# Kernel tuning notes

Hardware: AMD Instinct MI355X
Metric: run time of the kernel (lower is better)

## Reference

```python
import jax, jax.numpy as jnp
import numpy as np

CAL_W, BF_W, PCP_W, CX_W = 1.0, 1.0, 0.5, 0.5
LIQ_SCALE, EPS = 1.0, 1e-6
BIG = 1e30


def setup_inputs() -> dict:
    n_mat, n_str, W = 32, 256, 4
    N = n_mat * n_str
    rng = np.random.default_rng(0)
    lm = np.tile(np.linspace(-0.5, 0.5, n_str, dtype=np.float32), n_mat)
    tenor = np.repeat(np.linspace(0.02, 2.0, n_mat, dtype=np.float32), n_str)
    cp = (rng.random(N) > 0.5).astype(np.float32)
    geometry = np.stack([lm, tenor, cp], axis=1)
    liquidity = rng.standard_normal((N, 4)).astype(np.float32)
    predicted_iv = (0.1 + 0.5 * rng.random((N, 1))).astype(np.float32)
    node_embeddings = rng.standard_normal((N, 256)).astype(np.float32)
    node = np.arange(N, dtype=np.int32).reshape(n_mat, n_str)
    src_s, dst_s = [], []
    for k in range(1, W + 1):  # strikes k apart within each maturity
        src_s.append(node[:, :-k].ravel()); dst_s.append(node[:, k:].ravel())
    edge_index_strike = np.stack([np.concatenate(src_s), np.concatenate(dst_s)])
    edge_index_maturity = np.stack([node[:-1].ravel(), node[1:].ravel()])
    return {
        'node_embeddings': jnp.asarray(node_embeddings),
        'predicted_iv': jnp.asarray(predicted_iv),
        'geometry': jnp.asarray(geometry),
        'liquidity': jnp.asarray(liquidity),
        'edge_index_strike': jnp.asarray(edge_index_strike),
        'edge_index_maturity': jnp.asarray(edge_index_maturity),
        'max_degree': 2 * W,
    }


def _padded_neighbors(edge_index, N, D):
    # CSR-style padded neighbor lists: row i = all undirected neighbors of i, -1 pad.
    src, dst = edge_index[0], edge_index[1]
    owners = jnp.concatenate([src, dst])
    nbrs = jnp.concatenate([dst, src])
    order = jnp.argsort(owners)  # jax sort is stable -> preserves [dst|src] order
    own_s, nbr_s = owners[order], nbrs[order]
    start = jnp.searchsorted(own_s, jnp.arange(N, dtype=own_s.dtype))
    rank = jnp.arange(own_s.shape[0], dtype=jnp.int32) - start[own_s].astype(jnp.int32)
    return jnp.full((N, D), -1, dtype=jnp.int32).at[own_s, rank].set(nbr_s.astype(jnp.int32))


def _forward(node_embeddings, predicted_iv, geometry, liquidity, edge_index_strike, edge_index_maturity, max_degree):
    lm, tenor, cp = geometry[:, 0], geometry[:, 1], geometry[:, 2]
    lw = jax.nn.sigmoid(liquidity[:, 3] * LIQ_SCALE)
    tv = predicted_iv[:, 0] ** 2 * jnp.maximum(tenor, EPS)  # total variance w = iv^2 * tau
    N = lm.shape[0]
    is_call = cp > 0.5

    # --- calendar arbitrage: total variance nondecreasing in tenor over maturity edges
    ms, md = edge_index_maturity[0], edge_index_maturity[1]
    cvalid = tenor[ms] < tenor[md] - EPS
    cviol = jax.nn.relu(tv[ms] - tv[md])
    cw = jnp.minimum(lw[ms], lw[md])
    ncal = cvalid.sum()
    calendar = jnp.where(ncal > 0, jnp.where(cvalid, cw * cviol, 0.0).sum() / jnp.maximum(ncal, 1), 0.0)

    # --- padded call-neighborhoods over strike edges, sorted by log-moneyness
    nbr = _padded_neighbors(edge_index_strike, N, max_degree)  # [N, D]
    nbr_safe = jnp.maximum(nbr, 0)
    nvalid = (nbr >= 0) & is_call[nbr_safe]
    key = jnp.where(nvalid, lm[nbr_safe], jnp.inf)  # invalid entries pushed to the end
    order = jnp.argsort(key, axis=1)
    ns = jnp.take_along_axis(nbr_safe, order, axis=1)
    vs = jnp.take_along_axis(nvalid, order, axis=1)
    n1, n2, n3 = ns[:, :-2], ns[:, 1:-1], ns[:, 2:]  # consecutive sorted triplets
    trip = vs[:, 2:] & is_call[:, None]  # triplet fully valid iff 3rd slot valid
    lm1, lm2, lm3 = lm[n1], lm[n2], lm[n3]
    denom = lm3 - lm1 + EPS
    alpha = (lm3 - lm2) / denom
    beta = (lm2 - lm1) / denom
    w_pair = lw[:, None] * lw[n2]
    tcount = trip.sum()

    # --- butterfly: interpolated total variance must not exceed the middle node's
    bviol = jax.nn.relu(alpha * tv[n1] + beta * tv[n3] - tv[n2])
    butterfly = jnp.where(tcount > 0, jnp.where(trip, w_pair * bviol, 0.0).sum() / jnp.maximum(tcount, 1), 0.0)

    # --- convexity on embedding norms
    en = jnp.linalg.norm(node_embeddings, axis=1)
    xviol = jax.nn.relu(en[n2] - (alpha * en[n1] + (1.0 - alpha) * en[n3]))
    convexity = jnp.where(tcount > 0, jnp.where(trip, w_pair * xviol, 0.0).sum() / jnp.maximum(tcount, 1), 0.0)

    # --- put-call parity: nearest put in (lm, tenor) per call, sum-sq embedding dist
    is_put = cp < 0.5
    dist = (lm[:, None] - lm[None, :]) ** 2 + (tenor[:, None] - tenor[None, :]) ** 2  # [N, N]
    dist = jnp.where(is_put[None, :], dist, BIG)
    best = jnp.argmin(dist, axis=1)
    emb_d = jnp.sum((node_embeddings - node_embeddings[best]) ** 2, axis=1)
    n_calls, n_puts = is_call.sum(), is_put.sum()
    pcp = jnp.where((n_calls > 0) & (n_puts > 0),
                    jnp.where(is_call, lw * lw[best] * emb_d, 0.0).sum() / jnp.maximum(n_calls, 1), 0.0)

    total = CAL_W * calendar + BF_W * butterfly + PCP_W * pcp + CX_W * convexity
    # order matches the module's dict: calendar, butterfly, put_call, convexity, total
    return jnp.stack([calendar, butterfly, pcp, convexity, total])


def reference(node_embeddings, predicted_iv, geometry, liquidity, edge_index_strike, edge_index_maturity, max_degree):
    return _forward(node_embeddings, predicted_iv, geometry, liquidity, edge_index_strike, edge_index_maturity, max_degree)
```

## Files before the change

kernel.cpp:

```cpp
#include <hip/hip_runtime.h>
#include <math.h>

#define EPS 1e-6f
#define DMAX 8
#define HALFW (DMAX / 2)
#define PREB 1024
#define NSTR 256
#define TAG 0x5A7E0000u
typedef unsigned long long ull;

__device__ __forceinline__ float waveSumF(float v) {
    #pragma unroll
    for (int m = 1; m < 64; m <<= 1) v += __shfl_xor(v, m, 64);
    return v;
}
__device__ __forceinline__ int waveSumI(int v) {
    #pragma unroll
    for (int m = 1; m < 64; m <<= 1) v += __shfl_xor(v, m, 64);
    return v;
}
__device__ __forceinline__ float sigmoidf(float x) {
    return 1.0f / (1.0f + expf(-x));
}

__global__ void k_pre(const float* __restrict__ emb, const float* __restrict__ iv,
                      const float* __restrict__ geom, const float* __restrict__ liq,
                      const int* __restrict__ es, const int* __restrict__ em,
                      float* lwA, float* tvA, float* lmA, float* enA, int* cpA, int* nbr,
                      float* calPartF, int* calPartI, int* ncPart, int* npPart,
                      int* bestj,
                      int N, int ED, int Es, int Em, int n_mat) {
    const int lane = threadIdx.x & 63;

    if ((int)blockIdx.x < PREB) {
        const int tid = blockIdx.x * 256 + threadIdx.x;
        const int gsz = PREB * 256;

        int ic = 0, ip = 0;
        for (int i = tid; i < N; i += gsz) {
            float lm = geom[3*i], ten = geom[3*i+1], cp = geom[3*i+2];
            lmA[i] = lm;
            int c = (cp > 0.5f) ? 1 : 0;
            ic += c; ip += (cp < 0.5f) ? 1 : 0;
            cpA[i] = c;
            lwA[i] = sigmoidf(liq[4*i+3]);
            float v = iv[i];
            tvA[i] = v * v * fmaxf(ten, EPS);
        }

        const int wid = tid >> 6, nw = gsz >> 6, ED4 = ED >> 2;
        for (int r = wid; r < N; r += nw) {
            const float4* row = (const float4*)(emb + (size_t)r * ED);
            float s = 0.f;
            for (int t = lane; t < ED4; t += 64) {
                float4 a = row[t];
                s += a.x*a.x + a.y*a.y + a.z*a.z + a.w*a.w;
            }
            s = waveSumF(s);
            if (lane == 0) enA[r] = sqrtf(s);
        }

        float c = 0.f; int n = 0;
        for (int e = tid; e < Em; e += gsz) {
            int s = em[e], d = em[Em + e];
            float ts = geom[3*s+1], td = geom[3*d+1];
            if (ts < td - EPS) {
                n++;
                float ivs = iv[s], ivd = iv[d];
                float tvs = ivs*ivs*fmaxf(ts, EPS), tvd = ivd*ivd*fmaxf(td, EPS);
                float lws = sigmoidf(liq[4*s+3]), lwd = sigmoidf(liq[4*d+3]);
                c += fminf(lws, lwd) * fmaxf(tvs - tvd, 0.f);
            }
        }
        for (int e = tid; e < Es; e += gsz) {
            int s = es[e], d = es[Es + e];
            int k = d - s;
            if (k >= 1 && k <= HALFW) {
                nbr[s * DMAX + (HALFW + k - 1)] = (int)(TAG | (unsigned)d);
                nbr[d * DMAX + (HALFW - k)]     = (int)(TAG | (unsigned)s);
            }
        }

        __shared__ float sf[4];
        __shared__ int si[4][3];
        c = waveSumF(c); n = waveSumI(n);
        int sc = waveSumI(ic), sp = waveSumI(ip);
        int w = threadIdx.x >> 6;
        if (lane == 0) { sf[w] = c; si[w][0] = n; si[w][1] = sc; si[w][2] = sp; }
        __syncthreads();
        if (threadIdx.x == 0) {
            calPartF[blockIdx.x] = sf[0]+sf[1]+sf[2]+sf[3];
            calPartI[blockIdx.x] = si[0][0]+si[1][0]+si[2][0]+si[3][0];
            ncPart[blockIdx.x]   = si[0][1]+si[1][1]+si[2][1]+si[3][1];
            npPart[blockIdx.x]   = si[0][2]+si[1][2]+si[2][2]+si[3][2];
        }
        return;
    }

    __shared__ float colD2[NSTR];
    __shared__ int   colJ[NSTR];
    __shared__ float colLm[NSTR];
    const int m = (int)blockIdx.x - PREB;
    const int t = threadIdx.x;

    float tm = geom[3*(m*NSTR + t) + 1];
    float bD2 = INFINITY; int bJ = 0; float bLm = 0.f;
    for (int mp = 0; mp < n_mat; ++mp) {
        int j = mp*NSTR + t;
        float lj = geom[3*j], tj = geom[3*j+1], cp = geom[3*j+2];
        float dt = tm - tj;
        float d2 = __fmul_rn(dt, dt);
        if (cp < 0.5f && d2 < bD2) { bD2 = d2; bJ = j; bLm = lj; }
    }
    colD2[t] = bD2; colJ[t] = bJ; colLm[t] = bLm;
    __syncthreads();

    const int i = m*NSTR + t;
    float lmi = geom[3*i];
    ull bestkey = ~0ULL;
    for (int sp = 0; sp < NSTR; ++sp) {
        float dl = lmi - colLm[sp];
        float d  = __fadd_rn(__fmul_rn(dl, dl), colD2[sp]);
        ull key = ((ull)__float_as_uint(d) << 32) | (unsigned)colJ[sp];
        if (key < bestkey) bestkey = key;
    }
    bestj[i] = (int)(bestkey & 0xffffffffULL);
}

__global__ void k_post(const float* __restrict__ emb, const int* __restrict__ bestj,
                       const int* __restrict__ cpA, const float* __restrict__ lwA,
                       const float* __restrict__ tvA, const float* __restrict__ lmA,
                       const float* __restrict__ enA, const int* __restrict__ nbr,
                       float* pcpPart, float* bfPart, float* cxPart, int* tcPart,
                       int N, int ED, int nPcp) {
    __shared__ float sblk[4];
    __shared__ float sblk2[4];
    __shared__ int   sblkI[4];
    const int lane = threadIdx.x & 63;
    const int w    = threadIdx.x >> 6;

    if ((int)blockIdx.x < nPcp) {
        const int i = (blockIdx.x * 256 + threadIdx.x) >> 6;
        const int ED4 = ED >> 2;
        float contrib = 0.f;
        if (i < N && cpA[i]) {
            int b = bestj[i];
            const float4* ri = (const float4*)(emb + (size_t)i * ED);
            const float4* rb = (const float4*)(emb + (size_t)b * ED);
            float s = 0.f;
            for (int t = lane; t < ED4; t += 64) {
                float4 a = ri[t], c = rb[t];
                float dx = a.x-c.x, dy = a.y-c.y, dz = a.z-c.z, dw = a.w-c.w;
                s += dx*dx + dy*dy + dz*dz + dw*dw;
            }
            s = waveSumF(s);
            contrib = lwA[i] * lwA[b] * s;
        }
        if (lane == 0) sblk[w] = contrib;
        __syncthreads();
        if (threadIdx.x == 0)
            pcpPart[blockIdx.x] = sblk[0]+sblk[1]+sblk[2]+sblk[3];
    } else {
        int bb = (int)blockIdx.x - nPcp;
        int i = bb * 256 + threadIdx.x;
        float bf = 0.f, cx = 0.f; int tc = 0;
        if (i < N) {
            int ids[DMAX]; float key[DMAX]; int mv = 0;
            for (int slot = 0; slot < DMAX; slot++) {
                unsigned v = (unsigned)nbr[i * DMAX + slot];
                if ((v & 0xFFFF0000u) == TAG) {
                    int nb = (int)(v & 0xFFFFu);
                    if (cpA[nb]) {
                        float kk = lmA[nb];
                        int p = mv++;
                        while (p > 0 && key[p-1] > kk) { key[p] = key[p-1]; ids[p] = ids[p-1]; p--; }
                        key[p] = kk; ids[p] = nb;
                    }
                }
            }
            if (cpA[i] && mv >= 3) {
                float lwi = lwA[i];
                for (int j = 0; j + 2 < mv; j++) {
                    int n1 = ids[j], n2 = ids[j+1], n3 = ids[j+2];
                    float lm1 = key[j], lm2 = key[j+1], lm3 = key[j+2];
                    float denom = lm3 - lm1 + EPS;
                    float alpha = (lm3 - lm2) / denom;
                    float beta  = (lm2 - lm1) / denom;
                    float bviol = fmaxf(alpha * tvA[n1] + beta * tvA[n3] - tvA[n2], 0.f);
                    float xviol = fmaxf(enA[n2] - (alpha * enA[n1] + (1.0f - alpha) * enA[n3]), 0.f);
                    float wgt = lwi * lwA[n2];
                    bf += wgt * bviol; cx += wgt * xviol; tc++;
                }
            }
        }
        bf = waveSumF(bf); cx = waveSumF(cx); tc = waveSumI(tc);
        if (lane == 0) { sblk[w] = bf; sblk2[w] = cx; sblkI[w] = tc; }
        __syncthreads();
        if (threadIdx.x == 0) {
            bfPart[bb] = sblk[0]+sblk[1]+sblk[2]+sblk[3];
            cxPart[bb] = sblk2[0]+sblk2[1]+sblk2[2]+sblk2[3];
            tcPart[bb] = sblkI[0]+sblkI[1]+sblkI[2]+sblkI[3];
        }
    }
}

__global__ void k_fin(const float* __restrict__ calPartF, const int* __restrict__ calPartI,
                      const int* __restrict__ ncPart, const int* __restrict__ npPart,
                      const float* __restrict__ pcpPart, const float* __restrict__ bfPart,
                      const float* __restrict__ cxPart, const int* __restrict__ tcPart,
                      float* out, int nPcp, int nBtf) {
    const int lane = threadIdx.x & 63;
    const int w    = threadIdx.x >> 6;
    float cs = 0.f, ps = 0.f, bs = 0.f, xs = 0.f;
    int cc = 0, ncall = 0, nput = 0, ts = 0;
    for (int t = threadIdx.x; t < PREB; t += 256) {
        cs += calPartF[t]; cc += calPartI[t]; ncall += ncPart[t]; nput += npPart[t];
    }
    for (int t = threadIdx.x; t < nPcp; t += 256) ps += pcpPart[t];
    for (int t = threadIdx.x; t < nBtf; t += 256) {
        bs += bfPart[t]; xs += cxPart[t]; ts += tcPart[t];
    }
    cs = waveSumF(cs); ps = waveSumF(ps); bs = waveSumF(bs); xs = waveSumF(xs);
    cc = waveSumI(cc); ncall = waveSumI(ncall); nput = waveSumI(nput); ts = waveSumI(ts);
    __shared__ float fcs[4], fps[4], fbs[4], fxs[4];
    __shared__ int   fcc[4], fnc[4], fnp[4], fts[4];
    if (lane == 0) {
        fcs[w] = cs; fps[w] = ps; fbs[w] = bs; fxs[w] = xs;
        fcc[w] = cc; fnc[w] = ncall; fnp[w] = nput; fts[w] = ts;
    }
    __syncthreads();
    if (threadIdx.x == 0) {
        float calSum = fcs[0]+fcs[1]+fcs[2]+fcs[3];
        float pcpSum = fps[0]+fps[1]+fps[2]+fps[3];
        float bfSum  = fbs[0]+fbs[1]+fbs[2]+fbs[3];
        float cxSum  = fxs[0]+fxs[1]+fxs[2]+fxs[3];
        int   calCnt = fcc[0]+fcc[1]+fcc[2]+fcc[3];
        int   nCalls = fnc[0]+fnc[1]+fnc[2]+fnc[3];
        int   nPuts  = fnp[0]+fnp[1]+fnp[2]+fnp[3];
        int   tcount = fts[0]+fts[1]+fts[2]+fts[3];
        float cal = (calCnt > 0) ? calSum / (float)max(calCnt, 1) : 0.f;
        float bf  = (tcount > 0) ? bfSum / (float)tcount : 0.f;
        float cx  = (tcount > 0) ? cxSum / (float)tcount : 0.f;
        float pcp = (nCalls > 0 && nPuts > 0) ? pcpSum / (float)max(nCalls, 1) : 0.f;
        out[0] = cal; out[1] = bf; out[2] = pcp; out[3] = cx;
        out[4] = cal + bf + 0.5f * pcp + 0.5f * cx;
    }
}

extern "C" void kernel_launch(void* const* d_in, const int* in_sizes, int n_in,
                              void* d_out, int out_size, void* d_ws, size_t ws_size,
                              hipStream_t stream) {
    const float* emb  = (const float*)d_in[0];
    const float* iv   = (const float*)d_in[1];
    const float* geom = (const float*)d_in[2];
    const float* liq  = (const float*)d_in[3];
    const int*   es   = (const int*)d_in[4];
    const int*   em   = (const int*)d_in[5];

    const int N  = in_sizes[1];
    const int ED = in_sizes[0] / N;
    const int Es = in_sizes[4] / 2;
    const int Em = in_sizes[5] / 2;
    const int n_mat = N / NSTR;

    const int nPcp = (N + 3) / 4;
    const int nBtf = (N + 255) / 256;

    float* calPartF = (float*)d_ws;
    int*   calPartI = (int*)d_ws + PREB;
    int*   ncPart   = calPartI + PREB;
    int*   npPart   = ncPart + PREB;
    float* pcpPart  = (float*)(npPart + PREB);
    float* bfPart   = pcpPart + nPcp;
    float* cxPart   = bfPart + nBtf;
    int*   tcPart   = (int*)(cxPart + nBtf);
    float* lwA      = (float*)(tcPart + nBtf);
    float* tvA      = lwA + N;
    float* lmA      = tvA + N;
    float* enA      = lmA + N;
    int*   cpA      = (int*)(enA + N);
    int*   nbr      = cpA + N;
    int*   bestj    = nbr + (size_t)DMAX * N;

    k_pre<<<PREB + n_mat, 256, 0, stream>>>(
        emb, iv, geom, liq, es, em,
        lwA, tvA, lmA, enA, cpA, nbr,
        calPartF, calPartI, ncPart, npPart, bestj,
        N, ED, Es, Em, n_mat);

    k_post<<<nPcp + nBtf, 256, 0, stream>>>(
        emb, bestj, cpA, lwA, tvA, lmA, enA, nbr,
        pcpPart, bfPart, cxPart, tcPart, N, ED, nPcp);

    k_fin<<<1, 256, 0, stream>>>(
        calPartF, calPartI, ncPart, npPart, pcpPart, bfPart, cxPart, tcPart,
        (float*)d_out, nPcp, nBtf);
}
```

Before: 98.57 us.

## Fuse final reduction into post kernel via last-block ticket and shrink grids

Removes the separate single-block finalize kernel and instead has the last block of the post kernel, chosen through an atomic ticket counter, perform the global reduction and write the outputs. The counter is zeroed inside the pre kernel. The put-call parity stage now uses a fixed grid of 256 blocks that loop over nodes grid-stride, instead of one wave per node with about 2048 blocks, and the pre kernel's block count is halved. This saves one kernel launch and shrinks the partial arrays, at the cost of an atomic, memory fences and less parallelism per stage.

```diff
diff --git a/kernel.cpp b/kernel.cpp
--- a/kernel.cpp
+++ b/kernel.cpp
@@ -4,7 +4,8 @@
 #define EPS 1e-6f
 #define DMAX 8
 #define HALFW (DMAX / 2)
-#define PREB 1024
+#define PREB 512
+#define PCPB 256
 #define NSTR 256
 #define TAG 0x5A7E0000u
 typedef unsigned long long ull;
@@ -28,13 +29,15 @@
                       const int* __restrict__ es, const int* __restrict__ em,
                       float* lwA, float* tvA, float* lmA, float* enA, int* cpA, int* nbr,
                       float* calPartF, int* calPartI, int* ncPart, int* npPart,
-                      int* bestj,
+                      int* bestj, int* acc,
                       int N, int ED, int Es, int Em, int n_mat) {
     const int lane = threadIdx.x & 63;
 
     if ((int)blockIdx.x < PREB) {
         const int tid = blockIdx.x * 256 + threadIdx.x;
         const int gsz = PREB * 256;
+
+        if (blockIdx.x == 0 && threadIdx.x < 16) acc[threadIdx.x] = 0;
 
         int ic = 0, ip = 0;
         for (int i = tid; i < N; i += gsz) {
@@ -131,37 +134,43 @@
                        const int* __restrict__ cpA, const float* __restrict__ lwA,
                        const float* __restrict__ tvA, const float* __restrict__ lmA,
                        const float* __restrict__ enA, const int* __restrict__ nbr,
+                       const float* __restrict__ calPartF, const int* __restrict__ calPartI,
+                       const int* __restrict__ ncPart, const int* __restrict__ npPart,
                        float* pcpPart, float* bfPart, float* cxPart, int* tcPart,
-                       int N, int ED, int nPcp) {
+                       int* acc, float* out, int N, int ED, int nBtf) {
     __shared__ float sblk[4];
     __shared__ float sblk2[4];
     __shared__ int   sblkI[4];
+    __shared__ int   sticket;
     const int lane = threadIdx.x & 63;
     const int w    = threadIdx.x >> 6;
 
-    if ((int)blockIdx.x < nPcp) {
-        const int i = (blockIdx.x * 256 + threadIdx.x) >> 6;
+    if ((int)blockIdx.x < PCPB) {
+        const int gw = (blockIdx.x * 256 + threadIdx.x) >> 6;
+        const int nw = PCPB * 4;
         const int ED4 = ED >> 2;
-        float contrib = 0.f;
-        if (i < N && cpA[i]) {
-            int b = bestj[i];
-            const float4* ri = (const float4*)(emb + (size_t)i * ED);
-            const float4* rb = (const float4*)(emb + (size_t)b * ED);
-            float s = 0.f;
-            for (int t = lane; t < ED4; t += 64) {
-                float4 a = ri[t], c = rb[t];
-                float dx = a.x-c.x, dy = a.y-c.y, dz = a.z-c.z, dw = a.w-c.w;
-                s += dx*dx + dy*dy + dz*dz + dw*dw;
-            }
-            s = waveSumF(s);
-            contrib = lwA[i] * lwA[b] * s;
-        }
-        if (lane == 0) sblk[w] = contrib;
+        float wacc = 0.f;
+        for (int i = gw; i < N; i += nw) {
+            if (cpA[i]) {
+                int b = bestj[i];
+                const float4* ri = (const float4*)(emb + (size_t)i * ED);
+                const float4* rb = (const float4*)(emb + (size_t)b * ED);
+                float s = 0.f;
+                for (int t = lane; t < ED4; t += 64) {
+                    float4 a = ri[t], c = rb[t];
+                    float dx = a.x-c.x, dy = a.y-c.y, dz = a.z-c.z, dw = a.w-c.w;
+                    s += dx*dx + dy*dy + dz*dz + dw*dw;
+                }
+                s = waveSumF(s);
+                wacc += lwA[i] * lwA[b] * s;
+            }
+        }
+        if (lane == 0) sblk[w] = wacc;
         __syncthreads();
         if (threadIdx.x == 0)
             pcpPart[blockIdx.x] = sblk[0]+sblk[1]+sblk[2]+sblk[3];
     } else {
-        int bb = (int)blockIdx.x - nPcp;
+        int bb = (int)blockIdx.x - PCPB;
         int i = bb * 256 + threadIdx.x;
         float bf = 0.f, cx = 0.f; int tc = 0;
         if (i < N) {
@@ -202,48 +211,48 @@
             tcPart[bb] = sblkI[0]+sblkI[1]+sblkI[2]+sblkI[3];
         }
     }
-}
-
-__global__ void k_fin(const float* __restrict__ calPartF, const int* __restrict__ calPartI,
-                      const int* __restrict__ ncPart, const int* __restrict__ npPart,
-                      const float* __restrict__ pcpPart, const float* __restrict__ bfPart,
-                      const float* __restrict__ cxPart, const int* __restrict__ tcPart,
-                      float* out, int nPcp, int nBtf) {
-    const int lane = threadIdx.x & 63;
-    const int w    = threadIdx.x >> 6;
-    float cs = 0.f, ps = 0.f, bs = 0.f, xs = 0.f;
-    int cc = 0, ncall = 0, nput = 0, ts = 0;
-    for (int t = threadIdx.x; t < PREB; t += 256) {
-        cs += calPartF[t]; cc += calPartI[t]; ncall += ncPart[t]; nput += npPart[t];
-    }
-    for (int t = threadIdx.x; t < nPcp; t += 256) ps += pcpPart[t];
-    for (int t = threadIdx.x; t < nBtf; t += 256) {
-        bs += bfPart[t]; xs += cxPart[t]; ts += tcPart[t];
-    }
-    cs = waveSumF(cs); ps = waveSumF(ps); bs = waveSumF(bs); xs = waveSumF(xs);
-    cc = waveSumI(cc); ncall = waveSumI(ncall); nput = waveSumI(nput); ts = waveSumI(ts);
-    __shared__ float fcs[4], fps[4], fbs[4], fxs[4];
-    __shared__ int   fcc[4], fnc[4], fnp[4], fts[4];
-    if (lane == 0) {
-        fcs[w] = cs; fps[w] = ps; fbs[w] = bs; fxs[w] = xs;
-        fcc[w] = cc; fnc[w] = ncall; fnp[w] = nput; fts[w] = ts;
+
+    if (threadIdx.x == 0) {
+        __threadfence();
+        sticket = atomicAdd(&acc[9], 1);
     }
     __syncthreads();
-    if (threadIdx.x == 0) {
-        float calSum = fcs[0]+fcs[1]+fcs[2]+fcs[3];
-        float pcpSum = fps[0]+fps[1]+fps[2]+fps[3];
-        float bfSum  = fbs[0]+fbs[1]+fbs[2]+fbs[3];
-        float cxSum  = fxs[0]+fxs[1]+fxs[2]+fxs[3];
-        int   calCnt = fcc[0]+fcc[1]+fcc[2]+fcc[3];
-        int   nCalls = fnc[0]+fnc[1]+fnc[2]+fnc[3];
-        int   nPuts  = fnp[0]+fnp[1]+fnp[2]+fnp[3];
-        int   tcount = fts[0]+fts[1]+fts[2]+fts[3];
-        float cal = (calCnt > 0) ? calSum / (float)max(calCnt, 1) : 0.f;
-        float bf  = (tcount > 0) ? bfSum / (float)tcount : 0.f;
-        float cx  = (tcount > 0) ? cxSum / (float)tcount : 0.f;
-        float pcp = (nCalls > 0 && nPuts > 0) ? pcpSum / (float)max(nCalls, 1) : 0.f;
-        out[0] = cal; out[1] = bf; out[2] = pcp; out[3] = cx;
-        out[4] = cal + bf + 0.5f * pcp + 0.5f * cx;
+    if (sticket == (int)gridDim.x - 1) {
+        __threadfence();
+        float cs = 0.f, ps = 0.f, bs = 0.f, xs = 0.f;
+        int cc = 0, ncall = 0, nput = 0, ts = 0;
+        for (int t = threadIdx.x; t < PREB; t += 256) {
+            cs += calPartF[t]; cc += calPartI[t]; ncall += ncPart[t]; nput += npPart[t];
+        }
+        for (int t = threadIdx.x; t < PCPB; t += 256) ps += pcpPart[t];
+        for (int t = threadIdx.x; t < nBtf; t += 256) {
+            bs += bfPart[t]; xs += cxPart[t]; ts += tcPart[t];
+        }
+        cs = waveSumF(cs); ps = waveSumF(ps); bs = waveSumF(bs); xs = waveSumF(xs);
+        cc = waveSumI(cc); ncall = waveSumI(ncall); nput = waveSumI(nput); ts = waveSumI(ts);
+        __shared__ float fcs[4], fps[4], fbs[4], fxs[4];
+        __shared__ int   fcc[4], fnc[4], fnp[4], fts[4];
+        if (lane == 0) {
+            fcs[w] = cs; fps[w] = ps; fbs[w] = bs; fxs[w] = xs;
+            fcc[w] = cc; fnc[w] = ncall; fnp[w] = nput; fts[w] = ts;
+        }
+        __syncthreads();
+        if (threadIdx.x == 0) {
+            float calSum = fcs[0]+fcs[1]+fcs[2]+fcs[3];
+            float pcpSum = fps[0]+fps[1]+fps[2]+fps[3];
+            float bfSum  = fbs[0]+fbs[1]+fbs[2]+fbs[3];
+            float cxSum  = fxs[0]+fxs[1]+fxs[2]+fxs[3];
+            int   calCnt = fcc[0]+fcc[1]+fcc[2]+fcc[3];
+            int   nCalls = fnc[0]+fnc[1]+fnc[2]+fnc[3];
+            int   nPuts  = fnp[0]+fnp[1]+fnp[2]+fnp[3];
+            int   tcount = fts[0]+fts[1]+fts[2]+fts[3];
+            float cal = (calCnt > 0) ? calSum / (float)max(calCnt, 1) : 0.f;
+            float bf  = (tcount > 0) ? bfSum / (float)tcount : 0.f;
+            float cx  = (tcount > 0) ? cxSum / (float)tcount : 0.f;
+            float pcp = (nCalls > 0 && nPuts > 0) ? pcpSum / (float)max(nCalls, 1) : 0.f;
+            out[0] = cal; out[1] = bf; out[2] = pcp; out[3] = cx;
+            out[4] = cal + bf + 0.5f * pcp + 0.5f * cx;
+        }
     }
 }
 
@@ -262,16 +271,15 @@
     const int Es = in_sizes[4] / 2;
     const int Em = in_sizes[5] / 2;
     const int n_mat = N / NSTR;
-
-    const int nPcp = (N + 3) / 4;
-    const int nBtf = (N + 255) / 256;
-
-    float* calPartF = (float*)d_ws;
-    int*   calPartI = (int*)d_ws + PREB;
+    const int nBtf  = (N + 255) / 256;
+
+    int*   acc      = (int*)d_ws;
+    float* calPartF = (float*)d_ws + 16;
+    int*   calPartI = (int*)d_ws + 16 + PREB;
     int*   ncPart   = calPartI + PREB;
     int*   npPart   = ncPart + PREB;
     float* pcpPart  = (float*)(npPart + PREB);
-    float* bfPart   = pcpPart + nPcp;
+    float* bfPart   = pcpPart + PCPB;
     float* cxPart   = bfPart + nBtf;
     int*   tcPart   = (int*)(cxPart + nBtf);
     float* lwA      = (float*)(tcPart + nBtf);
@@ -285,14 +293,12 @@
     k_pre<<<PREB + n_mat, 256, 0, stream>>>(
         emb, iv, geom, liq, es, em,
         lwA, tvA, lmA, enA, cpA, nbr,
-        calPartF, calPartI, ncPart, npPart, bestj,
+        calPartF, calPartI, ncPart, npPart, bestj, acc,
         N, ED, Es, Em, n_mat);
 
-    k_post<<<nPcp + nBtf, 256, 0, stream>>>(
+    k_post<<<PCPB + nBtf, 256, 0, stream>>>(
         emb, bestj, cpA, lwA, tvA, lmA, enA, nbr,
-        pcpPart, bfPart, cxPart, tcPart, N, ED, nPcp);
-
-    k_fin<<<1, 256, 0, stream>>>(
-        calPartF, calPartI, ncPart, npPart, pcpPart, bfPart, cxPart, tcPart,
-        (float*)d_out, nPcp, nBtf);
-}
+        calPartF, calPartI, ncPart, npPart,
+        pcpPart, bfPart, cxPart, tcPart,
+        acc, (float*)d_out, N, ED, nBtf);
+}
```

Result: no change. 99.67 us (+1.1%).
